# Performance work log

Hardware: AMD Instinct MI355X
Metric: run time of the kernel (lower is better)

Reference implementation:

```python
import jax, jax.numpy as jnp
import numpy as np

# static conv hyperparams (match init_kwargs)
KH = KW = 3
SH = SW = 1
PH = PW = 1
DH = DW = 1


def _unfold(x):
    """torch F.unfold equivalent with constant pad value -1.
    x: (N, C, H, W) -> patches (N, C*KH*KW, L), feature order (C, kh, kw)."""
    N, C, H, W = x.shape
    H_out = (H + 2 * PH - DH * (KH - 1) - 1) // SH + 1
    W_out = (W + 2 * PW - DW * (KW - 1) - 1) // SW + 1
    padded = jnp.pad(x, ((0, 0), (0, 0), (PH, PH), (PW, PW)), constant_values=-1.0)
    cols = [
        padded[:, :, ih * DH: ih * DH + SH * H_out: SH,
                     iw * DW: iw * DW + SW * W_out: SW]
        for ih in range(KH) for iw in range(KW)
    ]
    patches = jnp.stack(cols, axis=2)  # (N, C, KH*KW, H_out, W_out)
    return patches.reshape(N, C * KH * KW, H_out * W_out), H_out, W_out


def _maj3_tree(x):
    """Recursive 3-way majority-gate tree reduction over the last axis.
    x: (..., K) with K a power of 3. MAJ3Fn math: xs=(x+1)/2;
    r = ab+ac+bc-2abc; y = 2r-1."""
    while x.shape[-1] > 1:
        k = x.shape[-1] // 3
        g = x.reshape(x.shape[:-1] + (k, 3))
        s = (g + 1.0) * 0.5
        a, b, c = s[..., 0], s[..., 1], s[..., 2]
        r = a * b + a * c + b * c - 2.0 * a * b * c
        x = 2.0 * r - 1.0
    return x[..., 0]


def setup_inputs() -> dict:
    key = jax.random.key(0)
    k1, k2 = jax.random.split(key)
    x = jax.random.normal(k1, (8, 27, 32, 32), dtype=jnp.float32)
    # kaiming_uniform-ish scale for (OC=27, C=27, 3, 3)
    fan_in = 27 * 3 * 3
    bound = np.sqrt(6.0 / fan_in)
    weight = jax.random.uniform(k2, (27, 27, 3, 3), dtype=jnp.float32,
                                minval=-bound, maxval=bound)
    return {"x": x, "weight": weight}


def reference(x, weight):
    N = x.shape[0]
    OC = weight.shape[0]
    patches, H_out, W_out = _unfold(x)          # (N, K, L), K = C*KH*KW
    wf = weight.reshape(OC, -1)                  # (OC, K)
    prod = patches[:, None, :, :] * wf[None, :, :, None]  # (N, OC, K, L)
    prod = jnp.moveaxis(prod, 2, -1)             # (N, OC, L, K)
    out = _maj3_tree(prod)                       # (N, OC, L)
    return out.reshape(N, OC, H_out, W_out)
```

## Files before the change

### kernel.cpp

```cpp
#include <hip/hip_runtime.h>


#define HH 32
#define WW 32
#define CC 27
#define OCC 27

__device__ __forceinline__ float maj3(float a, float b, float c) {
    float ab = a * b;
    float t  = fmaf(-2.0f, ab, a + b);
    return fmaf(c, t, ab);
}

__global__ __launch_bounds__(256) void sconv_maj_kernel(
    const float* __restrict__ x, const float* __restrict__ w, float* __restrict__ out)
{
    __shared__ float tile[270 * 36];

    const int b    = blockIdx.x;
    const int rg   = b & 3;
    const int rest = b >> 2;
    const int ocg  = rest % 7;
    const int n    = rest / 7;
    const int tid  = threadIdx.x;

    const float* __restrict__ xb = x + n * (CC * HH * WW);

    {
        const int lane = tid & 31;
        const int team = tid >> 5;
        for (int R = team; R < 270; R += 8) {
            const int c  = R / 10;
            const int tr = R - c * 10;
            const int ih = rg * 8 + tr - 1;
            float v = -0.5f;
            if ((unsigned)ih < 32u) v = 0.5f * xb[c * (HH * WW) + ih * WW + lane];
            tile[R * 36 + 1 + lane] = v;
        }
        for (int i = tid; i < 540; i += 256) {
            const int R = i >> 1;
            tile[R * 36 + ((i & 1) ? 33 : 0)] = -0.5f;
        }
    }
    __syncthreads();

    int oc = ocg * 4 + (tid >> 6);
    oc = __builtin_amdgcn_readfirstlane(oc);
    const int lt  = tid & 63;
    const int pr  = lt >> 3;
    const int ow0 = (lt & 7) << 2;

    if (oc < OCC) {
        const float* __restrict__ wp = w + oc * 243;
        const int tb = pr * 36 + ow0;

        float l5[3][4];
#pragma unroll
        for (int c3 = 0; c3 < 3; ++c3) {
            float l4[3][4];
#pragma unroll
            for (int c2 = 0; c2 < 3; ++c2) {
                float l3[3][4];
#pragma unroll
                for (int c1 = 0; c1 < 3; ++c1) {
                    const int c = c3 * 9 + c2 * 3 + c1;
                    const float* trow = &tile[c * 360 + tb];
                    float r[3][4];
#pragma unroll
                    for (int kh = 0; kh < 3; ++kh) {
                        const float4 u = *(const float4*)(trow + kh * 36);
                        const float2 v = *(const float2*)(trow + kh * 36 + 4);
                        const float t0 = u.x, t1 = u.y, t2 = u.z, t3 = u.w;
                        const float t4 = v.x, t5 = v.y;
                        const float w0 = wp[c * 9 + kh * 3 + 0];
                        const float w1 = wp[c * 9 + kh * 3 + 1];
                        const float w2 = wp[c * 9 + kh * 3 + 2];
                        r[kh][0] = maj3(fmaf(t0, w0, 0.5f), fmaf(t1, w1, 0.5f), fmaf(t2, w2, 0.5f));
                        r[kh][1] = maj3(fmaf(t1, w0, 0.5f), fmaf(t2, w1, 0.5f), fmaf(t3, w2, 0.5f));
                        r[kh][2] = maj3(fmaf(t2, w0, 0.5f), fmaf(t3, w1, 0.5f), fmaf(t4, w2, 0.5f));
                        r[kh][3] = maj3(fmaf(t3, w0, 0.5f), fmaf(t4, w1, 0.5f), fmaf(t5, w2, 0.5f));
                    }
#pragma unroll
                    for (int p = 0; p < 4; ++p)
                        l3[c1][p] = maj3(r[0][p], r[1][p], r[2][p]);
                }
#pragma unroll
                for (int p = 0; p < 4; ++p)
                    l4[c2][p] = maj3(l3[0][p], l3[1][p], l3[2][p]);
            }
#pragma unroll
            for (int p = 0; p < 4; ++p)
                l5[c3][p] = maj3(l4[0][p], l4[1][p], l4[2][p]);
        }
        float4 o;
        o.x = fmaf(2.0f, maj3(l5[0][0], l5[1][0], l5[2][0]), -1.0f);
        o.y = fmaf(2.0f, maj3(l5[0][1], l5[1][1], l5[2][1]), -1.0f);
        o.z = fmaf(2.0f, maj3(l5[0][2], l5[1][2], l5[2][2]), -1.0f);
        o.w = fmaf(2.0f, maj3(l5[0][3], l5[1][3], l5[2][3]), -1.0f);

        const int oh = rg * 8 + pr;
        *(float4*)(out + (((n * OCC + oc) * HH) + oh) * WW + ow0) = o;
    }
}

extern "C" void kernel_launch(void* const* d_in, const int* in_sizes, int n_in,
                              void* d_out, int out_size, void* d_ws, size_t ws_size,
                              hipStream_t stream) {
    const float* x = (const float*)d_in[0];
    const float* w = (const float*)d_in[1];
    float* out = (float*)d_out;
    sconv_maj_kernel<<<dim3(8 * 4 * 7), dim3(256), 0, stream>>>(x, w, out);
}
```

Before: 74.19 us.

## Split majority tree across nine waves per output channel with LDS combine

Each block now handles one output channel and row group with 9 wavefronts. Each wave reduces 3 input channels to a partial majority value and writes it to shared memory, and a final stage combines the 9 partials. The grid grows from 224 to 864 blocks, giving more parallelism and shorter per-thread dependency chains. The cost is that each block reloads the input tile for only one output channel (the old code shared it across four), plus an extra barrier and LDS round trip.

```diff
diff --git a/kernel.cpp b/kernel.cpp
--- a/kernel.cpp
+++ b/kernel.cpp
@@ -12,16 +12,17 @@
     return fmaf(c, t, ab);
 }
 
-__global__ __launch_bounds__(256) void sconv_maj_kernel(
+__global__ __launch_bounds__(576, 7) void sconv_maj_kernel(
     const float* __restrict__ x, const float* __restrict__ w, float* __restrict__ out)
 {
     __shared__ float tile[270 * 36];
+    __shared__ float part[9 * 256];
 
     const int b    = blockIdx.x;
     const int rg   = b & 3;
     const int rest = b >> 2;
-    const int ocg  = rest % 7;
-    const int n    = rest / 7;
+    const int oc   = rest % OCC;
+    const int n    = rest / OCC;
     const int tid  = threadIdx.x;
 
     const float* __restrict__ xb = x + n * (CC * HH * WW);
@@ -29,7 +30,7 @@
     {
         const int lane = tid & 31;
         const int team = tid >> 5;
-        for (int R = team; R < 270; R += 8) {
+        for (int R = team; R < 270; R += 18) {
             const int c  = R / 10;
             const int tr = R - c * 10;
             const int ih = rg * 8 + tr - 1;
@@ -37,69 +38,60 @@
             if ((unsigned)ih < 32u) v = 0.5f * xb[c * (HH * WW) + ih * WW + lane];
             tile[R * 36 + 1 + lane] = v;
         }
-        for (int i = tid; i < 540; i += 256) {
+        for (int i = tid; i < 540; i += 576) {
             const int R = i >> 1;
             tile[R * 36 + ((i & 1) ? 33 : 0)] = -0.5f;
         }
     }
     __syncthreads();
 
-    int oc = ocg * 4 + (tid >> 6);
-    oc = __builtin_amdgcn_readfirstlane(oc);
+    const int g   = __builtin_amdgcn_readfirstlane(tid >> 6);
     const int lt  = tid & 63;
     const int pr  = lt >> 3;
     const int ow0 = (lt & 7) << 2;
 
-    if (oc < OCC) {
-        const float* __restrict__ wp = w + oc * 243;
-        const int tb = pr * 36 + ow0;
-
-        float l5[3][4];
+    {
+        const float* __restrict__ wp = w + oc * 243 + g * 27;
+        float p3[4][3];
 #pragma unroll
-        for (int c3 = 0; c3 < 3; ++c3) {
-            float l4[3][4];
+        for (int c1 = 0; c1 < 3; ++c1) {
+            const int c = g * 3 + c1;
+            const float* trow = &tile[(c * 10 + pr) * 36 + ow0];
+            float rr[4][3];
 #pragma unroll
-            for (int c2 = 0; c2 < 3; ++c2) {
-                float l3[3][4];
-#pragma unroll
-                for (int c1 = 0; c1 < 3; ++c1) {
-                    const int c = c3 * 9 + c2 * 3 + c1;
-                    const float* trow = &tile[c * 360 + tb];
-                    float r[3][4];
-#pragma unroll
-                    for (int kh = 0; kh < 3; ++kh) {
-                        const float4 u = *(const float4*)(trow + kh * 36);
-                        const float2 v = *(const float2*)(trow + kh * 36 + 4);
-                        const float t0 = u.x, t1 = u.y, t2 = u.z, t3 = u.w;
-                        const float t4 = v.x, t5 = v.y;
-                        const float w0 = wp[c * 9 + kh * 3 + 0];
-                        const float w1 = wp[c * 9 + kh * 3 + 1];
-                        const float w2 = wp[c * 9 + kh * 3 + 2];
-                        r[kh][0] = maj3(fmaf(t0, w0, 0.5f), fmaf(t1, w1, 0.5f), fmaf(t2, w2, 0.5f));
-                        r[kh][1] = maj3(fmaf(t1, w0, 0.5f), fmaf(t2, w1, 0.5f), fmaf(t3, w2, 0.5f));
-                        r[kh][2] = maj3(fmaf(t2, w0, 0.5f), fmaf(t3, w1, 0.5f), fmaf(t4, w2, 0.5f));
-                        r[kh][3] = maj3(fmaf(t3, w0, 0.5f), fmaf(t4, w1, 0.5f), fmaf(t5, w2, 0.5f));
-                    }
-#pragma unroll
-                    for (int p = 0; p < 4; ++p)
-                        l3[c1][p] = maj3(r[0][p], r[1][p], r[2][p]);
-                }
-#pragma unroll
-                for (int p = 0; p < 4; ++p)
-                    l4[c2][p] = maj3(l3[0][p], l3[1][p], l3[2][p]);
+            for (int kh = 0; kh < 3; ++kh) {
+                const float4 u = *(const float4*)(trow + kh * 36);
+                const float2 v = *(const float2*)(trow + kh * 36 + 4);
+                const float w0 = wp[c1 * 9 + kh * 3 + 0];
+                const float w1 = wp[c1 * 9 + kh * 3 + 1];
+                const float w2 = wp[c1 * 9 + kh * 3 + 2];
+                rr[0][kh] = maj3(fmaf(u.x, w0, 0.5f), fmaf(u.y, w1, 0.5f), fmaf(u.z, w2, 0.5f));
+                rr[1][kh] = maj3(fmaf(u.y, w0, 0.5f), fmaf(u.z, w1, 0.5f), fmaf(u.w, w2, 0.5f));
+                rr[2][kh] = maj3(fmaf(u.z, w0, 0.5f), fmaf(u.w, w1, 0.5f), fmaf(v.x, w2, 0.5f));
+                rr[3][kh] = maj3(fmaf(u.w, w0, 0.5f), fmaf(v.x, w1, 0.5f), fmaf(v.y, w2, 0.5f));
             }
 #pragma unroll
             for (int p = 0; p < 4; ++p)
-                l5[c3][p] = maj3(l4[0][p], l4[1][p], l4[2][p]);
+                p3[p][c1] = maj3(rr[p][0], rr[p][1], rr[p][2]);
         }
         float4 o;
-        o.x = fmaf(2.0f, maj3(l5[0][0], l5[1][0], l5[2][0]), -1.0f);
-        o.y = fmaf(2.0f, maj3(l5[0][1], l5[1][1], l5[2][1]), -1.0f);
-        o.z = fmaf(2.0f, maj3(l5[0][2], l5[1][2], l5[2][2]), -1.0f);
-        o.w = fmaf(2.0f, maj3(l5[0][3], l5[1][3], l5[2][3]), -1.0f);
+        o.x = maj3(p3[0][0], p3[0][1], p3[0][2]);
+        o.y = maj3(p3[1][0], p3[1][1], p3[1][2]);
+        o.z = maj3(p3[2][0], p3[2][1], p3[2][2]);
+        o.w = maj3(p3[3][0], p3[3][1], p3[3][2]);
+        *(float4*)(&part[g * 256 + pr * 32 + ow0]) = o;
+    }
+    __syncthreads();
 
-        const int oh = rg * 8 + pr;
-        *(float4*)(out + (((n * OCC + oc) * HH) + oh) * WW + ow0) = o;
+    if (tid < 256) {
+        const int px = tid;
+        const float m0 = maj3(part[0 * 256 + px], part[1 * 256 + px], part[2 * 256 + px]);
+        const float m1 = maj3(part[3 * 256 + px], part[4 * 256 + px], part[5 * 256 + px]);
+        const float m2 = maj3(part[6 * 256 + px], part[7 * 256 + px], part[8 * 256 + px]);
+        const float y  = fmaf(2.0f, maj3(m0, m1, m2), -1.0f);
+        const int oh = rg * 8 + (px >> 5);
+        const int ow = px & 31;
+        out[(((n * OCC + oc) * HH) + oh) * WW + ow] = y;
     }
 }
 
@@ -109,5 +101,5 @@
     const float* x = (const float*)d_in[0];
     const float* w = (const float*)d_in[1];
     float* out = (float*)d_out;
-    sconv_maj_kernel<<<dim3(8 * 4 * 7), dim3(256), 0, stream>>>(x, w, out);
+    sconv_maj_kernel<<<dim3(8 * OCC * 4), dim3(576), 0, stream>>>(x, w, out);
 }
```

Result: no change. 74.37 us (+0.2%).
